# Performance work log

Hardware: AMD Instinct MI355X
Metric: run time of the kernel (lower is better)

## Reference

```python
import jax, jax.numpy as jnp
import numpy as np

N_GAUSS = 1024
IMG = 192
TANFOV = 0.5  # tan(FoV/2), both axes
ZNEAR, ZFAR = 0.01, 100.0

C0 = 0.28209479177387814
C1 = 0.4886025119029199
C2 = (1.0925484305920792, -1.0925484305920792, 0.31539156525252005, -1.0925484305920792, 0.5462742152960396)
C3 = (-0.5900435899266435, 2.890611442640554, -0.4570457994644658, 0.3731763325901154, -0.4570457994644658, 1.445305721320277, -0.5900435899266435)


def _eval_sh3(sh, d):
    # sh: [N,16,3] coeffs, d: [N,3] unit dirs -> clamped rgb [N,3]
    x, y, z = d[:, 0:1], d[:, 1:2], d[:, 2:3]
    xx, yy, zz = x * x, y * y, z * z
    xy, yz, xz = x * y, y * z, x * z
    res = (C0 * sh[:, 0]
           - C1 * y * sh[:, 1] + C1 * z * sh[:, 2] - C1 * x * sh[:, 3]
           + C2[0] * xy * sh[:, 4] + C2[1] * yz * sh[:, 5]
           + C2[2] * (2.0 * zz - xx - yy) * sh[:, 6]
           + C2[3] * xz * sh[:, 7] + C2[4] * (xx - yy) * sh[:, 8]
           + C3[0] * y * (3.0 * xx - yy) * sh[:, 9]
           + C3[1] * xy * z * sh[:, 10]
           + C3[2] * y * (4.0 * zz - xx - yy) * sh[:, 11]
           + C3[3] * z * (2.0 * zz - 3.0 * xx - 3.0 * yy) * sh[:, 12]
           + C3[4] * x * (4.0 * zz - xx - yy) * sh[:, 13]
           + C3[5] * z * (xx - yy) * sh[:, 14]
           + C3[6] * x * (xx - yy - 3.0 * zz) * sh[:, 15])
    return jnp.maximum(res + 0.5, 0.0)


def _quat_to_rot(q):
    r, x, y, z = q[:, 0], q[:, 1], q[:, 2], q[:, 3]
    return jnp.stack([
        1 - 2 * (y * y + z * z), 2 * (x * y - r * z), 2 * (x * z + r * y),
        2 * (x * y + r * z), 1 - 2 * (x * x + z * z), 2 * (y * z - r * x),
        2 * (x * z - r * y), 2 * (y * z + r * x), 1 - 2 * (x * x + y * y),
    ], axis=-1).reshape(-1, 3, 3)


def setup_inputs() -> dict:
    key = jax.random.key(0)
    ks = jax.random.split(key, 6)
    xy = jax.random.uniform(ks[0], (N_GAUSS, 2), minval=-2.0, maxval=2.0)
    z = jax.random.uniform(ks[1], (N_GAUSS, 1), minval=2.0, maxval=10.0)
    means3D = jnp.concatenate([xy, z], axis=1)
    scales = jax.random.uniform(ks[2], (N_GAUSS, 3), minval=0.01, maxval=0.08)
    q = jax.random.normal(ks[3], (N_GAUSS, 4))
    rotations = q / jnp.linalg.norm(q, axis=1, keepdims=True)
    opacities = jax.random.uniform(ks[4], (N_GAUSS, 1), minval=0.1, maxval=0.99)
    shs = jax.random.normal(ks[5], (N_GAUSS, 16, 3)) * 0.3
    viewmatrix = jnp.eye(4, dtype=jnp.float32)
    proj = np.zeros((4, 4), np.float32)
    proj[0, 0] = 1.0 / TANFOV
    proj[1, 1] = 1.0 / TANFOV
    proj[2, 2] = ZFAR / (ZFAR - ZNEAR)
    proj[2, 3] = -ZFAR * ZNEAR / (ZFAR - ZNEAR)
    proj[3, 2] = 1.0
    return dict(means3D=means3D, scales=scales, rotations=rotations,
                opacities=opacities, shs=shs, viewmatrix=viewmatrix,
                projmatrix=jnp.asarray(proj), campos=jnp.zeros(3, jnp.float32),
                bg_color=jnp.zeros(3, jnp.float32),
                image_height=IMG, image_width=IMG)


def reference(means3D, scales, rotations, opacities, shs, viewmatrix,
              projmatrix, campos, bg_color, image_height, image_width):
    H, W = int(image_height), int(image_width)
    fx = W / (2.0 * TANFOV)
    fy = H / (2.0 * TANFOV)
    N = means3D.shape[0]

    # SH -> RGB (convert_SHs_python branch, active_sh_degree = 3)
    dir_pp = means3D - campos[None, :]
    dir_pp = dir_pp / jnp.linalg.norm(dir_pp, axis=1, keepdims=True)
    colors = _eval_sh3(shs, dir_pp)  # [N,3]

    # 3D covariance Sigma = (R S)(R S)^T  (scale_modifier = 1.0)
    R = _quat_to_rot(rotations)
    M = R * scales[:, None, :]
    cov3d = jnp.einsum('nij,nkj->nik', M, M)  # [N,3,3]

    # projection of means
    hom = jnp.concatenate([means3D, jnp.ones((N, 1), means3D.dtype)], axis=1)
    p_view = hom @ viewmatrix.T
    depth = p_view[:, 2]
    p_hom = hom @ projmatrix.T
    p_proj = p_hom[:, :3] / (p_hom[:, 3:4] + 1e-7)
    gx = ((p_proj[:, 0] + 1.0) * W - 1.0) * 0.5  # ndc2Pix
    gy = ((p_proj[:, 1] + 1.0) * H - 1.0) * 0.5
    means2D = jnp.stack([gx, gy], axis=1)

    in_front = depth > 0.2
    tz = jnp.where(in_front, depth, 1.0)
    lim = 1.3 * TANFOV
    tx = jnp.clip(p_view[:, 0] / tz, -lim, lim) * tz
    ty = jnp.clip(p_view[:, 1] / tz, -lim, lim) * tz

    # EWA splatting: J (top 2 rows) composed with view rotation
    zeros = jnp.zeros_like(tz)
    J = jnp.stack([
        jnp.stack([fx / tz, zeros, -fx * tx / (tz * tz)], axis=-1),
        jnp.stack([zeros, fy / tz, -fy * ty / (tz * tz)], axis=-1),
    ], axis=1)  # [N,2,3]
    T = jnp.einsum('nij,jk->nik', J, viewmatrix[:3, :3])
    cov2d = jnp.einsum('nij,njk,nlk->nil', T, cov3d, T)  # [N,2,2]
    a = cov2d[:, 0, 0] + 0.3  # low-pass filter on diagonal
    b = cov2d[:, 0, 1]
    c = cov2d[:, 1, 1] + 0.3

    det = a * c - b * b
    pos_det = det > 0
    inv_det = jnp.where(pos_det, 1.0 / jnp.where(pos_det, det, 1.0), 0.0)
    conA, conB, conC = c * inv_det, -b * inv_det, a * inv_det

    mid = 0.5 * (a + c)
    lam = mid + jnp.sqrt(jnp.maximum(mid * mid - det, 0.1))
    visible = in_front & pos_det
    radii = jnp.where(visible, jnp.ceil(3.0 * jnp.sqrt(lam)), 0.0)
    visibility_filter = radii > 0

    # per-pixel depth-sorted alpha compositing (dense stand-in for tiles)
    yy, xx = jnp.meshgrid(jnp.arange(H, dtype=means3D.dtype),
                          jnp.arange(W, dtype=means3D.dtype), indexing='ij')
    px = xx.reshape(-1)
    py = yy.reshape(-1)
    dx = gx[None, :] - px[:, None]  # [P,N]
    dy = gy[None, :] - py[:, None]
    power = (-0.5 * (conA[None, :] * dx * dx + conC[None, :] * dy * dy)
             - conB[None, :] * dx * dy)
    keep = ((jnp.abs(dx) <= radii[None, :]) & (jnp.abs(dy) <= radii[None, :])
            & visible[None, :] & (power <= 0.0))
    alpha = jnp.minimum(0.99, opacities[:, 0][None, :] * jnp.exp(jnp.minimum(power, 0.0)))
    alpha = jnp.where(keep & (alpha >= 1.0 / 255.0), alpha, 0.0)

    order = jnp.argsort(jnp.where(visible, depth, jnp.inf))
    a_s = alpha[:, order]
    Tcum = jnp.cumprod(1.0 - a_s, axis=1)
    T_before = jnp.concatenate(
        [jnp.ones((a_s.shape[0], 1), a_s.dtype), Tcum[:, :-1]], axis=1)
    wgt = a_s * T_before
    img = wgt @ colors[order] + Tcum[:, -1:] * bg_color[None, :]
    rendered = img.reshape(H, W, 3).transpose(2, 0, 1)  # CHW like torch
    return rendered, radii.astype(jnp.int32), visibility_filter, means2D
```

## Files before the change

### kernel.cpp

```cpp
#include <hip/hip_runtime.h>

#define NG      1024
#define W_IMG   192
#define H_IMG   192
#define HW      (W_IMG * H_IMG)
#define PSTR    12
#define NSEG    8
#define SEGLEN  (NG / NSEG)
#define TILES_X (W_IMG / 8)
#define TILES_Y (H_IMG / 8)
#define NTILES  (TILES_X * TILES_Y)


__global__ __launch_bounds__(64) void preprocess_kernel(
    const float* __restrict__ means3D, const float* __restrict__ scales,
    const float* __restrict__ rotations, const float* __restrict__ opacities,
    const float* __restrict__ shs, const float* __restrict__ viewm,
    const float* __restrict__ projm, const float* __restrict__ campos,
    float* __restrict__ params, float* __restrict__ keys,
    float* __restrict__ outp)
{
    const int i = blockIdx.x * 64 + threadIdx.x;
    if (i >= NG) return;

    const float mx = means3D[i * 3 + 0];
    const float my = means3D[i * 3 + 1];
    const float mz = means3D[i * 3 + 2];

    float dxc = mx - campos[0], dyc = my - campos[1], dzc = mz - campos[2];
    float nrm = sqrtf(dxc * dxc + dyc * dyc + dzc * dzc);
    float x = dxc / nrm, y = dyc / nrm, z = dzc / nrm;
    float xx = x * x, yy = y * y, zz = z * z;
    float xy = x * y, yz = y * z, xz = x * z;

    float basis[16];
    basis[0]  = 0.28209479177387814f;
    basis[1]  = -0.4886025119029199f * y;
    basis[2]  =  0.4886025119029199f * z;
    basis[3]  = -0.4886025119029199f * x;
    basis[4]  =  1.0925484305920792f * xy;
    basis[5]  = -1.0925484305920792f * yz;
    basis[6]  =  0.31539156525252005f * (2.f * zz - xx - yy);
    basis[7]  = -1.0925484305920792f * xz;
    basis[8]  =  0.5462742152960396f * (xx - yy);
    basis[9]  = -0.5900435899266435f * y * (3.f * xx - yy);
    basis[10] =  2.890611442640554f  * xy * z;
    basis[11] = -0.4570457994644658f * y * (4.f * zz - xx - yy);
    basis[12] =  0.3731763325901154f * z * (2.f * zz - 3.f * xx - 3.f * yy);
    basis[13] = -0.4570457994644658f * x * (4.f * zz - xx - yy);
    basis[14] =  1.445305721320277f  * z * (xx - yy);
    basis[15] = -0.5900435899266435f * x * (xx - yy - 3.f * zz);

    float cr = 0.f, cg = 0.f, cb = 0.f;
#pragma unroll
    for (int k = 0; k < 16; ++k) {
        float b = basis[k];
        cr += b * shs[(i * 16 + k) * 3 + 0];
        cg += b * shs[(i * 16 + k) * 3 + 1];
        cb += b * shs[(i * 16 + k) * 3 + 2];
    }
    cr = fmaxf(cr + 0.5f, 0.f);
    cg = fmaxf(cg + 0.5f, 0.f);
    cb = fmaxf(cb + 0.5f, 0.f);

    float qr = rotations[i * 4 + 0], qx = rotations[i * 4 + 1];
    float qy = rotations[i * 4 + 2], qz = rotations[i * 4 + 3];
    float sx = scales[i * 3 + 0], sy = scales[i * 3 + 1], sz = scales[i * 3 + 2];
    float R00 = 1.f - 2.f * (qy * qy + qz * qz), R01 = 2.f * (qx * qy - qr * qz), R02 = 2.f * (qx * qz + qr * qy);
    float R10 = 2.f * (qx * qy + qr * qz), R11 = 1.f - 2.f * (qx * qx + qz * qz), R12 = 2.f * (qy * qz - qr * qx);
    float R20 = 2.f * (qx * qz - qr * qy), R21 = 2.f * (qy * qz + qr * qx), R22 = 1.f - 2.f * (qx * qx + qy * qy);
    float M00 = R00 * sx, M01 = R01 * sy, M02 = R02 * sz;
    float M10 = R10 * sx, M11 = R11 * sy, M12 = R12 * sz;
    float M20 = R20 * sx, M21 = R21 * sy, M22 = R22 * sz;
    float S00 = M00 * M00 + M01 * M01 + M02 * M02;
    float S01 = M00 * M10 + M01 * M11 + M02 * M12;
    float S02 = M00 * M20 + M01 * M21 + M02 * M22;
    float S11 = M10 * M10 + M11 * M11 + M12 * M12;
    float S12 = M10 * M20 + M11 * M21 + M12 * M22;
    float S22 = M20 * M20 + M21 * M21 + M22 * M22;

    float pv0 = viewm[0] * mx + viewm[1] * my + viewm[2]  * mz + viewm[3];
    float pv1 = viewm[4] * mx + viewm[5] * my + viewm[6]  * mz + viewm[7];
    float pv2 = viewm[8] * mx + viewm[9] * my + viewm[10] * mz + viewm[11];
    float ph0 = projm[0]  * mx + projm[1]  * my + projm[2]  * mz + projm[3];
    float ph1 = projm[4]  * mx + projm[5]  * my + projm[6]  * mz + projm[7];
    float ph3 = projm[12] * mx + projm[13] * my + projm[14] * mz + projm[15];
    float pp0 = ph0 / (ph3 + 1e-7f);
    float pp1 = ph1 / (ph3 + 1e-7f);
    float gx = ((pp0 + 1.f) * (float)W_IMG - 1.f) * 0.5f;
    float gy = ((pp1 + 1.f) * (float)H_IMG - 1.f) * 0.5f;

    float depth = pv2;
    bool in_front = depth > 0.2f;
    float tz = in_front ? depth : 1.f;
    const float lim = 1.3f * 0.5f;
    float txv = fminf(fmaxf(pv0 / tz, -lim), lim) * tz;
    float tyv = fminf(fmaxf(pv1 / tz, -lim), lim) * tz;
    const float fx = (float)W_IMG / (2.f * 0.5f);
    const float fy = (float)H_IMG / (2.f * 0.5f);
    float J00 = fx / tz, J02 = -fx * txv / (tz * tz);
    float J11 = fy / tz, J12 = -fy * tyv / (tz * tz);

    float T00 = J00 * viewm[0] + J02 * viewm[8];
    float T01 = J00 * viewm[1] + J02 * viewm[9];
    float T02 = J00 * viewm[2] + J02 * viewm[10];
    float T10 = J11 * viewm[4] + J12 * viewm[8];
    float T11 = J11 * viewm[5] + J12 * viewm[9];
    float T12 = J11 * viewm[6] + J12 * viewm[10];

    float u0 = T00 * S00 + T01 * S01 + T02 * S02;
    float u1 = T00 * S01 + T01 * S11 + T02 * S12;
    float u2 = T00 * S02 + T01 * S12 + T02 * S22;
    float v0 = T10 * S00 + T11 * S01 + T12 * S02;
    float v1 = T10 * S01 + T11 * S11 + T12 * S12;
    float v2 = T10 * S02 + T11 * S12 + T12 * S22;
    float c00 = u0 * T00 + u1 * T01 + u2 * T02;
    float c01 = u0 * T10 + u1 * T11 + u2 * T12;
    float c11 = v0 * T10 + v1 * T11 + v2 * T12;

    float a = c00 + 0.3f;
    float b = c01;
    float c = c11 + 0.3f;
    float det = a * c - b * b;
    bool pos_det = det > 0.f;
    float inv_det = pos_det ? 1.f / det : 0.f;
    float conA = c * inv_det, conB = -b * inv_det, conC = a * inv_det;
    float mid = 0.5f * (a + c);
    float lam = mid + sqrtf(fmaxf(mid * mid - det, 0.1f));
    bool visible = in_front && pos_det;
    float radii = visible ? ceilf(3.f * sqrtf(lam)) : 0.f;

    float opa = opacities[i];

    outp[3 * HW + i] = radii;
    outp[3 * HW + NG + i] = (radii > 0.f) ? 1.f : 0.f;
    outp[3 * HW + 2 * NG + i * 2 + 0] = gx;
    outp[3 * HW + 2 * NG + i * 2 + 1] = gy;

    float* p = params + i * PSTR;
    p[0] = gx;   p[1] = gy;   p[2]  = radii; p[3]  = visible ? opa : 0.f;
    p[4] = conA; p[5] = conB; p[6]  = conC;  p[7]  = 0.f;
    p[8] = cr;   p[9] = cg;   p[10] = cb;    p[11] = 0.f;

    keys[i] = visible ? depth : 1e30f;
}

__global__ __launch_bounds__(64) void sort_kernel(
    const float* __restrict__ keys, const float* __restrict__ params,
    float* __restrict__ sorted)
{
    const int i = blockIdx.x;
    const int lane = threadIdx.x;
    const float ki = keys[i];
    int cnt = 0;
#pragma unroll
    for (int k = 0; k < NG / 64; ++k) {
        int j = lane + k * 64;
        float kj = keys[j];
        cnt += (kj < ki || (kj == ki && j < i)) ? 1 : 0;
    }
    for (int off = 32; off > 0; off >>= 1) cnt += __shfl_down(cnt, off);
    int rank = __shfl(cnt, 0);
    if (lane < PSTR) sorted[rank * PSTR + lane] = params[i * PSTR + lane];
}

__global__ __launch_bounds__(256) void raster_seg_kernel(
    const float* __restrict__ sorted, float4* __restrict__ segbuf)
{
    __shared__ float4 sp[SEGLEN * 3];
    const int t = threadIdx.x;
    const int tg  = blockIdx.x % (NTILES / 4);
    const int seg = blockIdx.x / (NTILES / 4);

    {
        const float4* src = (const float4*)(sorted + seg * SEGLEN * PSTR);
        for (int k = t; k < SEGLEN * 3; k += 256) sp[k] = src[k];
    }
    __syncthreads();

    const int wave = t >> 6;
    const int lane = t & 63;
    const int tileIdx = tg * 4 + wave;
    const int tileX = tileIdx % TILES_X;
    const int tileY = tileIdx / TILES_X;
    const int lx = lane & 7, ly = lane >> 3;
    const int pxi = tileX * 8 + lx;
    const int pyi = tileY * 8 + ly;
    const float px = (float)pxi, py = (float)pyi;

    float T = 1.f, accR = 0.f, accG = 0.f, accB = 0.f;

    for (int j = 0; j < SEGLEN; ++j) {
        float4 g0 = sp[j * 3 + 0];
        float dx = g0.x - px, dy = g0.y - py;
        bool cover = (fabsf(dx) <= g0.z) && (fabsf(dy) <= g0.z);
        if (__any(cover)) {
            float4 g1 = sp[j * 3 + 1];
            float power = -0.5f * (g1.x * dx * dx + g1.z * dy * dy) - g1.y * dx * dy;
            float alpha = fminf(0.99f, g0.w * __expf(fminf(power, 0.f)));
            bool keep = cover && (power <= 0.f) && (alpha >= (1.f / 255.f));
            alpha = keep ? alpha : 0.f;
            float w = alpha * T;
            float4 g2 = sp[j * 3 + 2];
            accR += w * g2.x;
            accG += w * g2.y;
            accB += w * g2.z;
            T *= (1.f - alpha);
        }
    }

    const int pix = pyi * W_IMG + pxi;
    segbuf[seg * HW + pix] = make_float4(accR, accG, accB, T);
}

__global__ __launch_bounds__(256) void combine_kernel(
    const float4* __restrict__ segbuf, const float* __restrict__ bg,
    float* __restrict__ outp)
{
    const int pix = blockIdx.x * 256 + threadIdx.x;
    if (pix >= HW) return;
    float T = 1.f, r = 0.f, g = 0.f, b = 0.f;
#pragma unroll
    for (int s = 0; s < NSEG; ++s) {
        float4 c = segbuf[s * HW + pix];
        r += T * c.x;
        g += T * c.y;
        b += T * c.z;
        T *= c.w;
    }
    outp[pix]          = r + T * bg[0];
    outp[HW + pix]     = g + T * bg[1];
    outp[2 * HW + pix] = b + T * bg[2];
}

extern "C" void kernel_launch(void* const* d_in, const int* in_sizes, int n_in,
                              void* d_out, int out_size, void* d_ws, size_t ws_size,
                              hipStream_t stream)
{
    const float* means3D   = (const float*)d_in[0];
    const float* scales    = (const float*)d_in[1];
    const float* rotations = (const float*)d_in[2];
    const float* opacities = (const float*)d_in[3];
    const float* shs       = (const float*)d_in[4];
    const float* viewm     = (const float*)d_in[5];
    const float* projm     = (const float*)d_in[6];
    const float* campos    = (const float*)d_in[7];
    const float* bg        = (const float*)d_in[8];

    float* outp   = (float*)d_out;
    float* params = (float*)d_ws;
    float* sorted = params + NG * PSTR;
    float* keys   = sorted + NG * PSTR;
    float4* segbuf = (float4*)(keys + NG);

    preprocess_kernel<<<NG / 64, 64, 0, stream>>>(
        means3D, scales, rotations, opacities, shs, viewm, projm, campos,
        params, keys, outp);

    sort_kernel<<<NG, 64, 0, stream>>>(keys, params, sorted);

    raster_seg_kernel<<<(NTILES / 4) * NSEG, 256, 0, stream>>>(sorted, segbuf);

    combine_kernel<<<(HW + 255) / 256, 256, 0, stream>>>(segbuf, bg, outp);
}
```

Baseline: 93.78 us.

## Fuse segment raster and combine into one tile kernel with ballot culling

```diff
diff --git a/kernel.cpp b/kernel.cpp
--- a/kernel.cpp
+++ b/kernel.cpp
@@ -164,44 +164,60 @@
     if (lane < PSTR) sorted[rank * PSTR + lane] = params[i * PSTR + lane];
 }
 
-__global__ __launch_bounds__(256) void raster_seg_kernel(
-    const float* __restrict__ sorted, float4* __restrict__ segbuf)
-{
-    __shared__ float4 sp[SEGLEN * 3];
+__global__ __launch_bounds__(512) void raster_kernel(
+    const float* __restrict__ sorted, const float* __restrict__ bg,
+    float* __restrict__ outp)
+{
+    __shared__ float4 sp[NG * 3];
+    __shared__ float4 segacc[NSEG * 64];
+
     const int t = threadIdx.x;
-    const int tg  = blockIdx.x % (NTILES / 4);
-    const int seg = blockIdx.x / (NTILES / 4);
-
     {
-        const float4* src = (const float4*)(sorted + seg * SEGLEN * PSTR);
-        for (int k = t; k < SEGLEN * 3; k += 256) sp[k] = src[k];
+        const float4* src = (const float4*)sorted;
+        for (int k = t; k < NG * 3; k += 512) sp[k] = src[k];
     }
     __syncthreads();
 
     const int wave = t >> 6;
     const int lane = t & 63;
-    const int tileIdx = tg * 4 + wave;
-    const int tileX = tileIdx % TILES_X;
-    const int tileY = tileIdx / TILES_X;
+    const int tileX = blockIdx.x % TILES_X;
+    const int tileY = blockIdx.x / TILES_X;
     const int lx = lane & 7, ly = lane >> 3;
     const int pxi = tileX * 8 + lx;
     const int pyi = tileY * 8 + ly;
     const float px = (float)pxi, py = (float)pyi;
+    const float tx0 = (float)(tileX * 8);
+    const float ty0 = (float)(tileY * 8);
+
+    const int base = wave * SEGLEN;
+
+    unsigned long long m[2];
+#pragma unroll
+    for (int h = 0; h < 2; ++h) {
+        float4 g0 = sp[(base + h * 64 + lane) * 3];
+        bool hit = (g0.x >= tx0 - g0.z) && (g0.x <= tx0 + 7.f + g0.z) &&
+                   (g0.y >= ty0 - g0.z) && (g0.y <= ty0 + 7.f + g0.z);
+        m[h] = __ballot(hit);
+    }
 
     float T = 1.f, accR = 0.f, accG = 0.f, accB = 0.f;
-
-    for (int j = 0; j < SEGLEN; ++j) {
-        float4 g0 = sp[j * 3 + 0];
-        float dx = g0.x - px, dy = g0.y - py;
-        bool cover = (fabsf(dx) <= g0.z) && (fabsf(dy) <= g0.z);
-        if (__any(cover)) {
-            float4 g1 = sp[j * 3 + 1];
+#pragma unroll
+    for (int h = 0; h < 2; ++h) {
+        unsigned long long mask = m[h];
+        while (mask) {
+            const int j = __ffsll(mask) - 1;
+            mask &= mask - 1;
+            const int gi = base + h * 64 + j;
+            float4 g0 = sp[gi * 3 + 0];
+            float4 g1 = sp[gi * 3 + 1];
+            float4 g2 = sp[gi * 3 + 2];
+            float dx = g0.x - px, dy = g0.y - py;
+            bool cover = (fabsf(dx) <= g0.z) && (fabsf(dy) <= g0.z);
             float power = -0.5f * (g1.x * dx * dx + g1.z * dy * dy) - g1.y * dx * dy;
             float alpha = fminf(0.99f, g0.w * __expf(fminf(power, 0.f)));
             bool keep = cover && (power <= 0.f) && (alpha >= (1.f / 255.f));
             alpha = keep ? alpha : 0.f;
             float w = alpha * T;
-            float4 g2 = sp[j * 3 + 2];
             accR += w * g2.x;
             accG += w * g2.y;
             accB += w * g2.z;
@@ -209,28 +225,24 @@
         }
     }
 
-    const int pix = pyi * W_IMG + pxi;
-    segbuf[seg * HW + pix] = make_float4(accR, accG, accB, T);
-}
-
-__global__ __launch_bounds__(256) void combine_kernel(
-    const float4* __restrict__ segbuf, const float* __restrict__ bg,
-    float* __restrict__ outp)
-{
-    const int pix = blockIdx.x * 256 + threadIdx.x;
-    if (pix >= HW) return;
-    float T = 1.f, r = 0.f, g = 0.f, b = 0.f;
-#pragma unroll
-    for (int s = 0; s < NSEG; ++s) {
-        float4 c = segbuf[s * HW + pix];
-        r += T * c.x;
-        g += T * c.y;
-        b += T * c.z;
-        T *= c.w;
-    }
-    outp[pix]          = r + T * bg[0];
-    outp[HW + pix]     = g + T * bg[1];
-    outp[2 * HW + pix] = b + T * bg[2];
+    segacc[wave * 64 + lane] = make_float4(accR, accG, accB, T);
+    __syncthreads();
+
+    if (t < 64) {
+        float Tc = 1.f, r = 0.f, g = 0.f, b = 0.f;
+#pragma unroll
+        for (int s = 0; s < NSEG; ++s) {
+            float4 cc = segacc[s * 64 + t];
+            r += Tc * cc.x;
+            g += Tc * cc.y;
+            b += Tc * cc.z;
+            Tc *= cc.w;
+        }
+        const int pix = pyi * W_IMG + pxi;
+        outp[pix]          = r + Tc * bg[0];
+        outp[HW + pix]     = g + Tc * bg[1];
+        outp[2 * HW + pix] = b + Tc * bg[2];
+    }
 }
 
 extern "C" void kernel_launch(void* const* d_in, const int* in_sizes, int n_in,
@@ -251,7 +263,6 @@
     float* params = (float*)d_ws;
     float* sorted = params + NG * PSTR;
     float* keys   = sorted + NG * PSTR;
-    float4* segbuf = (float4*)(keys + NG);
 
     preprocess_kernel<<<NG / 64, 64, 0, stream>>>(
         means3D, scales, rotations, opacities, shs, viewm, projm, campos,
@@ -259,7 +270,5 @@
 
     sort_kernel<<<NG, 64, 0, stream>>>(keys, params, sorted);
 
-    raster_seg_kernel<<<(NTILES / 4) * NSEG, 256, 0, stream>>>(sorted, segbuf);
-
-    combine_kernel<<<(HW + 255) / 256, 256, 0, stream>>>(segbuf, bg, outp);
-}
+    raster_kernel<<<NTILES, 512, 0, stream>>>(sorted, bg, outp);
+}
```

Measured after the change: 85.18 us. 9.2% less time.
